# Performance work log

Measured on AMD Instinct MI355X. Metric: run time of the kernel, lower is better.

## Reference

```python
import jax, jax.numpy as jnp
import numpy as np

N, K, D, CP, H, S, P = 8192, 32, 768, 128, 8, 64, 8
NPTS = 3 * P  # 2*query_points + value_points = 24 points per head
FEAT = H * CP + H * S + H * P * 3 + H * P  # 1792


def layer_norm(x, scale, offset, eps=1e-5):
    m = x.mean(-1, keepdims=True)
    v = ((x - m) ** 2).mean(-1, keepdims=True)
    return (x - m) * jax.lax.rsqrt(v + eps) * scale + offset


def frames_from_pos(pos):
    # Gram-Schmidt rigid frame from backbone N(0), CA(1), C(2) atoms (extract_aa_frames).
    n, ca, c = pos[:, 0], pos[:, 1], pos[:, 2]
    eps = 1e-8
    v1 = c - ca
    v2 = n - ca
    e1 = v1 * jax.lax.rsqrt((v1 ** 2).sum(-1, keepdims=True) + eps)
    u2 = v2 - (v2 * e1).sum(-1, keepdims=True) * e1
    e2 = u2 * jax.lax.rsqrt((u2 ** 2).sum(-1, keepdims=True) + eps)
    e3 = jnp.cross(e1, e2)
    R = jnp.stack([e1, e2, e3], axis=-1)  # [N,3,3], columns = frame axes
    return R, ca


def setup_inputs() -> dict:
    key = jax.random.key(0)
    ks = jax.random.split(key, 10)
    inp = {
        "local": jax.random.normal(ks[0], (N, D), jnp.float32),
        "pos": jax.random.normal(ks[1], (N, 14, 3), jnp.float32) * 3.0,
        "pair": jax.random.normal(ks[2], (N, K, CP), jnp.float32),
        "pair_mask": jnp.ones((N, K), bool),
        "neighbours": jax.random.randint(ks[3], (N, K), 0, N, dtype=jnp.int32),
        "resi": jnp.arange(N, dtype=jnp.int32),
        "chain": jnp.zeros((N,), jnp.int32),
        "batch": jnp.zeros((N,), jnp.int32),
        "mask": jnp.ones((N,), bool),
        # parameters
        "ln_local_s": jnp.ones((D,), jnp.float32),
        "ln_local_b": jnp.zeros((D,), jnp.float32),
        "W_qkv": jax.random.normal(ks[4], (D, H * 3 * S), jnp.float32) / np.sqrt(D),
        "ln_q_s": jnp.ones((S,), jnp.float32),
        "ln_q_b": jnp.zeros((S,), jnp.float32),
        "ln_k_s": jnp.ones((S,), jnp.float32),
        "ln_k_b": jnp.zeros((S,), jnp.float32),
        "W_pts": jax.random.normal(ks[5], (D, H * NPTS * 3), jnp.float32) / np.sqrt(D),
        "W_bias": jax.random.normal(ks[6], (CP, H), jnp.float32) / np.sqrt(CP),
        "gamma": jnp.full((H,), np.log(np.e - 1.0), jnp.float32),
        "W_out": jax.random.normal(ks[7], (FEAT, D), jnp.float32) / np.sqrt(FEAT),
        "b_out": jnp.zeros((D,), jnp.float32),
    }
    return inp


def reference(local, pos, pair, pair_mask, neighbours, resi, chain, batch, mask,
              ln_local_s, ln_local_b, W_qkv, ln_q_s, ln_q_b, ln_k_s, ln_k_b,
              W_pts, W_bias, gamma, W_out, b_out):
    R, t = frames_from_pos(pos)                       # [N,3,3], [N,3]
    x = layer_norm(local, ln_local_s, ln_local_b)     # normalize=True
    qkv = (x @ W_qkv).reshape(-1, H, 3 * S)
    q, k, v = jnp.split(qkv, 3, axis=-1)              # each [N,H,S]
    q = layer_norm(q, ln_q_s, ln_q_b)
    k = layer_norm(k, ln_k_s, ln_k_b)
    # points in global frame: p = R @ raw + t
    raw = (x @ W_pts).reshape(-1, H, NPTS, 3)
    pts = jnp.einsum('nij,nhpj->nhpi', R, raw) + t[:, None, None]
    q_g, k_g, v_g = jnp.split(pts, [P, 2 * P], axis=-2)  # [N,H,P,3] each
    bias = jnp.einsum('nkc,ch->nkh', pair, W_bias)
    w_C = jnp.sqrt(2.0 / (9.0 * P))
    w_L = jnp.sqrt(1.0 / 3.0)
    dfactor = jax.nn.softplus(gamma)[None, None] * w_C / 2.0  # [1,1,H]
    diff = q_g[:, None] - k_g[neighbours]              # [N,K,H,P,3]
    dist = dfactor * (diff ** 2).sum((-1, -2))         # [N,K,H]
    dot = jnp.sqrt(1.0 / S) * jnp.einsum('nhc,nkhc->nkh', q, k[neighbours])
    logits = w_L * (dot + bias - dist)
    pm = pair_mask & (neighbours != -1)
    logits = jnp.where(pm[..., None], logits, -1e9)
    attn = jax.nn.softmax(logits, axis=1)              # softmax over neighbours (axis=-2)
    attn = jnp.where(pm[..., None], attn, 0.0)
    out_pair = jnp.einsum('nkh,nkc->nhc', attn, pair)
    out_scalar = jnp.einsum('nkh,nkhc->nhc', attn, v[neighbours])
    op = jnp.einsum('nkh,nkhpc->nhpc', attn, v_g[neighbours])
    # back to local frame: R^T (p - t)
    op = jnp.einsum('nji,nhpj->nhpi', R, op - t[:, None, None])
    out_norm = jnp.sqrt((op ** 2).sum(-1) + 1e-8)      # [N,H,P]
    Nn = local.shape[0]
    feats = jnp.concatenate([
        out_pair.reshape(Nn, -1), out_scalar.reshape(Nn, -1),
        op.reshape(Nn, -1), out_norm.reshape(Nn, -1)], axis=-1)
    return feats @ W_out + b_out
```

## Files before the change

### kernel.cpp

```cpp
#include <hip/hip_runtime.h>
#include <hip/hip_bf16.h>


#define NN 8192
#define KNBR 32
#define DD 768
#define CPC 128
#define HH 8
#define FEATD 1792
#define QKVD 1536
#define PTSD 576
#define PAIR_ROW 4096

typedef __hip_bfloat16 bf16;
typedef __attribute__((ext_vector_type(8))) short s8;
typedef __attribute__((ext_vector_type(4))) float f4;
typedef __attribute__((ext_vector_type(4))) float fv4;

__device__ __forceinline__ float b2f(bf16 v) { return __bfloat162float(v); }
__device__ __forceinline__ bf16 f2b(float v) { return __float2bfloat16(v); }
__device__ __forceinline__ unsigned short f2u(float v) {
    bf16 h = __float2bfloat16(v);
    return *(unsigned short*)&h;
}
__device__ __forceinline__ void gl_lds16(const void* g, void* l) {
    __builtin_amdgcn_global_load_lds(
        (const __attribute__((address_space(1))) void*)g,
        (__attribute__((address_space(3))) void*)l, 16, 0, 0);
}

__global__ __launch_bounds__(256) void frames_kernel(const float* __restrict__ pos,
                                                     float* __restrict__ Rm,
                                                     float* __restrict__ tv) {
    int n = blockIdx.x * blockDim.x + threadIdx.x;
    if (n >= NN) return;
    const float* p = pos + (size_t)n * 42;
    float nx[3], ca[3], cc[3];
#pragma unroll
    for (int j = 0; j < 3; ++j) { nx[j] = p[j]; ca[j] = p[3+j]; cc[j] = p[6+j]; }
    float v1[3], v2[3], e1[3], e2[3], e3[3];
#pragma unroll
    for (int j = 0; j < 3; ++j) { v1[j] = cc[j] - ca[j]; v2[j] = nx[j] - ca[j]; }
    float s1 = v1[0]*v1[0] + v1[1]*v1[1] + v1[2]*v1[2];
    float r1 = 1.0f / sqrtf(s1 + 1e-8f);
#pragma unroll
    for (int j = 0; j < 3; ++j) e1[j] = v1[j] * r1;
    float d = v2[0]*e1[0] + v2[1]*e1[1] + v2[2]*e1[2];
    float u2[3];
#pragma unroll
    for (int j = 0; j < 3; ++j) u2[j] = v2[j] - d * e1[j];
    float s2 = u2[0]*u2[0] + u2[1]*u2[1] + u2[2]*u2[2];
    float r2 = 1.0f / sqrtf(s2 + 1e-8f);
#pragma unroll
    for (int j = 0; j < 3; ++j) e2[j] = u2[j] * r2;
    e3[0] = e1[1]*e2[2] - e1[2]*e2[1];
    e3[1] = e1[2]*e2[0] - e1[0]*e2[2];
    e3[2] = e1[0]*e2[1] - e1[1]*e2[0];
#pragma unroll
    for (int i = 0; i < 3; ++i) {
        Rm[(size_t)n*9 + i*3 + 0] = e1[i];
        Rm[(size_t)n*9 + i*3 + 1] = e2[i];
        Rm[(size_t)n*9 + i*3 + 2] = e3[i];
        tv[(size_t)n*3 + i] = ca[i];
    }
}

__global__ __launch_bounds__(256) void ln_apply_kernel(const float* __restrict__ local,
                                                       const float* __restrict__ lns,
                                                       const float* __restrict__ lnb,
                                                       bf16* __restrict__ xln) {
    int n = blockIdx.x, tid = threadIdx.x;
    const float* row = local + (size_t)n * DD;
    float v[3];
#pragma unroll
    for (int e = 0; e < 3; ++e) v[e] = row[tid + 256*e];
    __shared__ float red[256];
    red[tid] = v[0] + v[1] + v[2];
    __syncthreads();
    for (int st = 128; st > 0; st >>= 1) {
        if (tid < st) red[tid] += red[tid + st];
        __syncthreads();
    }
    float mean = red[0] * (1.0f / DD);
    __syncthreads();
    float d0 = v[0]-mean, d1 = v[1]-mean, d2 = v[2]-mean;
    red[tid] = d0*d0 + d1*d1 + d2*d2;
    __syncthreads();
    for (int st = 128; st > 0; st >>= 1) {
        if (tid < st) red[tid] += red[tid + st];
        __syncthreads();
    }
    float rstd = rsqrtf(red[0] * (1.0f / DD) + 1e-5f);
    bf16* orow = xln + (size_t)n * DD;
#pragma unroll
    for (int e = 0; e < 3; ++e) {
        int c = tid + 256*e;
        orow[c] = f2b((v[e] - mean) * rstd * lns[c] + lnb[c]);
    }
}

__global__ __launch_bounds__(256) void transpose_kernel(const float* __restrict__ W,
                                                        bf16* __restrict__ Wt,
                                                        int K, int N,
                                                        int group, int cn, int segsz,
                                                        int rowoff) {
    __shared__ bf16 tile[32][33];
    int n0 = blockIdx.x * 32, k0 = blockIdx.y * 32;
    int tid = threadIdx.x;
    int r = tid >> 5, c = tid & 31;
    for (int rr = r; rr < 32; rr += 8) {
        int n = n0 + c;
        tile[rr][c] = (n < N) ? f2b(W[(size_t)(k0 + rr) * N + n]) : f2b(0.0f);
    }
    __syncthreads();
    for (int rr = r; rr < 32; rr += 8) {
        int n = n0 + rr;
        int pn = n;
        if (cn != 0 && n < N) {
            int hh = n / group, rm = n % group;
            pn = (rm / cn) * segsz + hh * cn + (rm % cn);
        }
        Wt[(size_t)(rowoff + pn) * K + k0 + c] = tile[c][rr];
    }
}

template<int SPLIT, int BIAS>
__global__ __launch_bounds__(256) void mfma_gemm(const bf16* __restrict__ A, int lda,
                                                 const bf16* __restrict__ Bt, int K,
                                                 void* __restrict__ C,
                                                 void* __restrict__ C2,
                                                 int ldc, int ncols,
                                                 const float* __restrict__ bias) {
    __shared__ short As[128 * 32];
    __shared__ short Bs[128 * 32];
    int tid = threadIdx.x;
    int w = tid >> 6, lane = tid & 63;
    int q = lane >> 4, lr = lane & 15;
    int m0 = blockIdx.y * 128, n0 = blockIdx.x * 128;
    int lrow = lane >> 2, lcol = (lane & 3) * 8;

    f4 acc[4][4] = {};

    for (int k0 = 0; k0 < K; k0 += 32) {
#pragma unroll
        for (int i = 0; i < 2; ++i) {
            int c = w * 2 + i;
            int r = c * 16 + lrow;
            gl_lds16(A  + (size_t)(m0 + r) * lda + k0 + lcol, As + c * 512);
            gl_lds16(Bt + (size_t)(n0 + r) * K   + k0 + lcol, Bs + c * 512);
        }
        __syncthreads();

        const short* Ab = As + ((w & 1) * 64 + lr) * 32 + q * 8;
        const short* Bb = Bs + ((w >> 1) * 64 + lr) * 32 + q * 8;
        s8 af[4], bfr[4];
#pragma unroll
        for (int i = 0; i < 4; ++i) af[i] = *(const s8*)(Ab + i * 16 * 32);
#pragma unroll
        for (int j = 0; j < 4; ++j) bfr[j] = *(const s8*)(Bb + j * 16 * 32);
#pragma unroll
        for (int i = 0; i < 4; ++i)
#pragma unroll
            for (int j = 0; j < 4; ++j)
                acc[i][j] = __builtin_amdgcn_mfma_f32_16x16x32_bf16(
                    af[i], bfr[j], acc[i][j], 0, 0, 0);
        __syncthreads();
    }

    int mb = m0 + (w & 1) * 64, nb = n0 + (w >> 1) * 64;
#pragma unroll
    for (int i = 0; i < 4; ++i) {
#pragma unroll
        for (int j = 0; j < 4; ++j) {
            int col = nb + j * 16 + lr;
            int row0 = mb + i * 16 + q * 4;
            if (!SPLIT) {
                if (col < ncols) {
#pragma unroll
                    for (int r = 0; r < 4; ++r) {
                        float v = acc[i][j][r];
                        if (BIAS) v += bias[col];
                        ((float*)C)[(size_t)(row0 + r) * ldc + col] = v;
                    }
                }
            } else {
                if (col < QKVD) {
#pragma unroll
                    for (int r = 0; r < 4; ++r)
                        ((unsigned short*)C)[(size_t)(row0 + r) * QKVD + col] =
                            f2u(acc[i][j][r]);
                } else if (col - QKVD < PTSD) {
                    int pc = col - QKVD;
#pragma unroll
                    for (int r = 0; r < 4; ++r)
                        ((float*)C2)[(size_t)(row0 + r) * PTSD + pc] = acc[i][j][r];
                }
            }
        }
    }
}

__global__ __launch_bounds__(256) void ln_qk_kernel(bf16* __restrict__ qkv,
                                                    const float* __restrict__ qs,
                                                    const float* __restrict__ qb,
                                                    const float* __restrict__ ks,
                                                    const float* __restrict__ kb) {
    int tid = threadIdx.x;
    int pi = blockIdx.x * 4 + (tid >> 6);
    int lane = tid & 63;
    bf16* base = qkv + (size_t)(pi >> 3) * QKVD + (pi & 7) * 64;
#pragma unroll
    for (int part = 0; part < 2; ++part) {
        int off = part * 512;
        const float* sc = part ? ks : qs;
        const float* of = part ? kb : qb;
        float v = b2f(base[off + lane]);
        float s = v;
#pragma unroll
        for (int m = 32; m > 0; m >>= 1) s += __shfl_xor(s, m, 64);
        float mean = s * (1.0f / 64.0f);
        float d = v - mean;
        float sq = d * d;
#pragma unroll
        for (int m = 32; m > 0; m >>= 1) sq += __shfl_xor(sq, m, 64);
        float inv = rsqrtf(sq * (1.0f / 64.0f) + 1e-5f);
        base[off + lane] = f2b(d * inv * sc[lane] + of[lane]);
    }
}

__global__ __launch_bounds__(256) void rotate_pts_kernel(float* __restrict__ pts,
                                                         const float* __restrict__ Rm,
                                                         const float* __restrict__ tv) {
    int idx = blockIdx.x * blockDim.x + threadIdx.x;
    if (idx >= NN * 192) return;
    int n = idx / 192;
    int rem = idx % 192;
    float* base = pts + (size_t)n * PTSD + rem * 3;
    float r0 = base[0], r1 = base[1], r2 = base[2];
    const float* R = Rm + (size_t)n * 9;
    const float* t = tv + (size_t)n * 3;
    base[0] = R[0]*r0 + R[1]*r1 + R[2]*r2 + t[0];
    base[1] = R[3]*r0 + R[4]*r1 + R[5]*r2 + t[1];
    base[2] = R[6]*r0 + R[7]*r1 + R[8]*r2 + t[2];
}

__global__ __launch_bounds__(256) void attn_kernel(const bf16* __restrict__ qkv,
                                                   const float* __restrict__ pts,
                                                   const float* __restrict__ Rm,
                                                   const float* __restrict__ tv,
                                                   float* __restrict__ pair,
                                                   const int* __restrict__ nbr,
                                                   const float* __restrict__ Wb,
                                                   const float* __restrict__ gamma) {
    int n = blockIdx.x;
    int tid = threadIdx.x;
    int w = tid >> 6, lane = tid & 63;
    int h = lane >> 3, cg = lane & 7;

    __shared__ float pairS[32][132];
    __shared__ float logitS[32][8];
    __shared__ float attnS[32][8];
    __shared__ float gS[192];
    __shared__ int nbS[32];
    __shared__ float dfS[8];

    const fv4* pr4 = (const fv4*)(pair + (size_t)n * PAIR_ROW);
    for (int e = tid; e < 1024; e += 256) {
        fv4 u = __builtin_nontemporal_load(pr4 + e);
        int k = e >> 5, c0 = (e & 31) * 4;
        *(fv4*)&pairS[k][c0] = u;
    }
    if (tid < 32) nbS[tid] = nbr[(size_t)n * KNBR + tid];
    if (tid < 8) dfS[tid] = log1pf(expf(gamma[tid])) * (1.0f / 12.0f);

    float qreg[8];
    {
        uint4 qv = *(const uint4*)(qkv + (size_t)n * QKVD + h * 64 + cg * 8);
        const unsigned short* qs = (const unsigned short*)&qv;
#pragma unroll
        for (int j = 0; j < 8; ++j) qreg[j] = b2f(*(const bf16*)&qs[j]);
    }
    fv4 qg = (fv4)(0.0f);
    if (cg < 6) qg = *(const fv4*)(pts + (size_t)n * PTSD + h * 24 + cg * 4);
    float wb[16];
#pragma unroll
    for (int j = 0; j < 16; ++j) wb[j] = Wb[(cg + 8 * j) * 8 + h];

    __syncthreads();

#pragma unroll
    for (int kk = 0; kk < 8; ++kk) {
        int k = w * 8 + kk;
        int nb = nbS[k];
        uint4 kv = *(const uint4*)(qkv + (size_t)nb * QKVD + 512 + h * 64 + cg * 8);
        const unsigned short* ks = (const unsigned short*)&kv;
        float dot = 0.0f;
#pragma unroll
        for (int j = 0; j < 8; ++j) dot += qreg[j] * b2f(*(const bf16*)&ks[j]);
        float d2 = 0.0f;
        if (cg < 6) {
            fv4 kg = *(const fv4*)(pts + (size_t)nb * PTSD + 192 + h * 24 + cg * 4);
            float dx = qg.x - kg.x, dy = qg.y - kg.y, dz = qg.z - kg.z, dw = qg.w - kg.w;
            d2 = dx*dx + dy*dy + dz*dz + dw*dw;
        }
        float bias = 0.0f;
#pragma unroll
        for (int j = 0; j < 16; ++j) bias += pairS[k][cg + 8 * j] * wb[j];

        float val = 0.125f * dot + bias - dfS[h] * d2;
        val += __shfl_xor(val, 1, 64);
        val += __shfl_xor(val, 2, 64);
        val += __shfl_xor(val, 4, 64);
        if (cg == 0) logitS[k][h] = 0.5773502691896258f * val;
    }
    __syncthreads();

    if (tid < 64) {
        int hh = tid >> 3, j = tid & 7;
        float l[4];
        float m = -1e30f;
#pragma unroll
        for (int i = 0; i < 4; ++i) { l[i] = logitS[j + 8 * i][hh]; m = fmaxf(m, l[i]); }
        m = fmaxf(m, __shfl_xor(m, 1, 64));
        m = fmaxf(m, __shfl_xor(m, 2, 64));
        m = fmaxf(m, __shfl_xor(m, 4, 64));
        float s = 0.0f;
#pragma unroll
        for (int i = 0; i < 4; ++i) { l[i] = expf(l[i] - m); s += l[i]; }
        s += __shfl_xor(s, 1, 64);
        s += __shfl_xor(s, 2, 64);
        s += __shfl_xor(s, 4, 64);
        float inv = 1.0f / s;
#pragma unroll
        for (int i = 0; i < 4; ++i) attnS[j + 8 * i][hh] = l[i] * inv;
    }
    __syncthreads();

    bf16* fr = (bf16*)(pair + (size_t)n * PAIR_ROW);
    for (int e = tid; e < 1024; e += 256) {
        int hh = e >> 7, c = e & 127;
        float acc = 0.0f;
#pragma unroll
        for (int k = 0; k < KNBR; ++k) acc += attnS[k][hh] * pairS[k][c];
        fr[e] = f2b(acc);
    }
    for (int e = tid; e < 512; e += 256) {
        int hh = e >> 6, c = e & 63;
        float acc = 0.0f;
#pragma unroll
        for (int k = 0; k < KNBR; ++k)
            acc += attnS[k][hh] * b2f(qkv[(size_t)nbS[k] * QKVD + 1024 + hh * 64 + c]);
        fr[1024 + e] = f2b(acc);
    }
    if (tid < 192) {
        int hh = tid / 24;
        float acc = 0.0f;
#pragma unroll
        for (int k = 0; k < KNBR; ++k)
            acc += attnS[k][hh] * pts[(size_t)nbS[k] * PTSD + 384 + tid];
        gS[tid] = acc;
    }
    __syncthreads();
    if (tid < 64) {
        int hh = tid >> 3, p = tid & 7;
        const float* t = tv + (size_t)n * 3;
        const float* R = Rm + (size_t)n * 9;
        float gx = gS[hh * 24 + p * 3 + 0] - t[0];
        float gy = gS[hh * 24 + p * 3 + 1] - t[1];
        float gz = gS[hh * 24 + p * 3 + 2] - t[2];
        float o0 = R[0]*gx + R[3]*gy + R[6]*gz;
        float o1 = R[1]*gx + R[4]*gy + R[7]*gz;
        float o2 = R[2]*gx + R[5]*gy + R[8]*gz;
        fr[1536 + hh*24 + p*3 + 0] = f2b(o0);
        fr[1536 + hh*24 + p*3 + 1] = f2b(o1);
        fr[1536 + hh*24 + p*3 + 2] = f2b(o2);
        fr[1728 + hh*8 + p] = f2b(sqrtf(o0*o0 + o1*o1 + o2*o2 + 1e-8f));
    }
}

extern "C" void kernel_launch(void* const* d_in, const int* in_sizes, int n_in,
                              void* d_out, int out_size, void* d_ws, size_t ws_size,
                              hipStream_t stream) {
    const float* local      = (const float*)d_in[0];
    const float* pos        = (const float*)d_in[1];
    float*       pair       = (float*)d_in[2];
    const int*   neighbours = (const int*)d_in[4];
    const float* ln_s   = (const float*)d_in[9];
    const float* ln_b   = (const float*)d_in[10];
    const float* W_qkv  = (const float*)d_in[11];
    const float* ln_q_s = (const float*)d_in[12];
    const float* ln_q_b = (const float*)d_in[13];
    const float* ln_k_s = (const float*)d_in[14];
    const float* ln_k_b = (const float*)d_in[15];
    const float* W_pts  = (const float*)d_in[16];
    const float* W_bias = (const float*)d_in[17];
    const float* gamma  = (const float*)d_in[18];
    const float* W_out  = (const float*)d_in[19];
    const float* b_out  = (const float*)d_in[20];
    float* out = (float*)d_out;

    float* Rm   = (float*)d_ws;
    float* tv   = Rm   + (size_t)NN * 9;
    float* pts  = tv   + (size_t)NN * 3;
    bf16*  qkv  = (bf16*)(pts + (size_t)NN * PTSD);
    bf16*  xln  = (bf16*)d_out;
    bf16*  wtm  = xln + (size_t)NN * DD;
    bf16*  wt3  = (bf16*)pts;

    frames_kernel<<<NN / 256, 256, 0, stream>>>(pos, Rm, tv);
    ln_apply_kernel<<<NN, 256, 0, stream>>>(local, ln_s, ln_b, xln);

    transpose_kernel<<<dim3(1536 / 32, 768 / 32), 256, 0, stream>>>(
        W_qkv, wtm, 768, 1536, 192, 64, 512, 0);
    transpose_kernel<<<dim3(640 / 32, 768 / 32), 256, 0, stream>>>(
        W_pts, wtm, 768, PTSD, 72, 24, 192, 1536);

    mfma_gemm<1, 0><<<dim3(2176 / 128, NN / 128), 256, 0, stream>>>(
        xln, DD, wtm, DD, qkv, pts, 0, 2176, nullptr);

    ln_qk_kernel<<<(NN * HH) / 4, 256, 0, stream>>>(qkv, ln_q_s, ln_q_b, ln_k_s, ln_k_b);
    rotate_pts_kernel<<<(NN * 192) / 256, 256, 0, stream>>>(pts, Rm, tv);

    attn_kernel<<<NN, 256, 0, stream>>>(qkv, pts, Rm, tv, pair, neighbours,
                                        W_bias, gamma);

    transpose_kernel<<<dim3(768 / 32, 1792 / 32), 256, 0, stream>>>(
        W_out, wt3, FEATD, DD, 0, 0, 0, 0);
    mfma_gemm<0, 1><<<dim3(768 / 128, NN / 128), 256, 0, stream>>>(
        (const bf16*)pair, PAIR_ROW * 2, wt3, FEATD, out, nullptr, DD, DD, b_out);
}
```

Before: 526.6 us.

## Fuse prep kernels, fold q/k layernorm into GEMM epilogue, vectorize pair aggregation

Frames, input layernorm and both weight transposes are merged into one prep launch, so four kernel launches become one. The separate q/k layernorm pass is removed: it now runs in the QKV GEMM epilogue using cross-lane shuffles over each 64-wide head tile, which saves a read-modify-write of the qkv buffer. The pair-feature aggregation in attention now computes four channels per thread with packed bf16 stores. The trade-offs are more divergent epilogue code and layernorm statistics taken from fp32 accumulators rather than from bf16-rounded values.

```diff
diff --git a/kernel.cpp b/kernel.cpp
--- a/kernel.cpp
+++ b/kernel.cpp
@@ -29,11 +29,9 @@
         (__attribute__((address_space(3))) void*)l, 16, 0, 0);
 }
 
-__global__ __launch_bounds__(256) void frames_kernel(const float* __restrict__ pos,
-                                                     float* __restrict__ Rm,
-                                                     float* __restrict__ tv) {
-    int n = blockIdx.x * blockDim.x + threadIdx.x;
-    if (n >= NN) return;
+__device__ __forceinline__ void do_frames(int n, const float* __restrict__ pos,
+                                          float* __restrict__ Rm,
+                                          float* __restrict__ tv) {
     const float* p = pos + (size_t)n * 42;
     float nx[3], ca[3], cc[3];
 #pragma unroll
@@ -65,48 +63,14 @@
     }
 }
 
-__global__ __launch_bounds__(256) void ln_apply_kernel(const float* __restrict__ local,
-                                                       const float* __restrict__ lns,
-                                                       const float* __restrict__ lnb,
-                                                       bf16* __restrict__ xln) {
-    int n = blockIdx.x, tid = threadIdx.x;
-    const float* row = local + (size_t)n * DD;
-    float v[3];
-#pragma unroll
-    for (int e = 0; e < 3; ++e) v[e] = row[tid + 256*e];
-    __shared__ float red[256];
-    red[tid] = v[0] + v[1] + v[2];
-    __syncthreads();
-    for (int st = 128; st > 0; st >>= 1) {
-        if (tid < st) red[tid] += red[tid + st];
-        __syncthreads();
-    }
-    float mean = red[0] * (1.0f / DD);
-    __syncthreads();
-    float d0 = v[0]-mean, d1 = v[1]-mean, d2 = v[2]-mean;
-    red[tid] = d0*d0 + d1*d1 + d2*d2;
-    __syncthreads();
-    for (int st = 128; st > 0; st >>= 1) {
-        if (tid < st) red[tid] += red[tid + st];
-        __syncthreads();
-    }
-    float rstd = rsqrtf(red[0] * (1.0f / DD) + 1e-5f);
-    bf16* orow = xln + (size_t)n * DD;
-#pragma unroll
-    for (int e = 0; e < 3; ++e) {
-        int c = tid + 256*e;
-        orow[c] = f2b((v[e] - mean) * rstd * lns[c] + lnb[c]);
-    }
-}
-
-__global__ __launch_bounds__(256) void transpose_kernel(const float* __restrict__ W,
-                                                        bf16* __restrict__ Wt,
-                                                        int K, int N,
-                                                        int group, int cn, int segsz,
-                                                        int rowoff) {
-    __shared__ bf16 tile[32][33];
-    int n0 = blockIdx.x * 32, k0 = blockIdx.y * 32;
-    int tid = threadIdx.x;
+__device__ __forceinline__ void do_transpose(const float* __restrict__ W,
+                                             bf16* __restrict__ Wt,
+                                             int K, int N, int group, int cn,
+                                             int segsz, int rowoff,
+                                             int bx, int by, int tid,
+                                             char* shbuf) {
+    bf16 (*tile)[33] = (bf16(*)[33])shbuf;
+    int n0 = bx * 32, k0 = by * 32;
     int r = tid >> 5, c = tid & 31;
     for (int rr = r; rr < 32; rr += 8) {
         int n = n0 + c;
@@ -124,13 +88,76 @@
     }
 }
 
+__global__ __launch_bounds__(256) void prep_kernel(
+        const float* __restrict__ local, const float* __restrict__ lns,
+        const float* __restrict__ lnb, bf16* __restrict__ xln,
+        const float* __restrict__ pos, float* __restrict__ Rm,
+        float* __restrict__ tv,
+        const float* __restrict__ W_qkv, const float* __restrict__ W_pts,
+        bf16* __restrict__ wtm) {
+    __shared__ __align__(16) char shbuf[2560];
+    int b = blockIdx.x, tid = threadIdx.x;
+    if (b < NN) {
+        if (b < 32) do_frames(b * 256 + tid, pos, Rm, tv);
+        float* red = (float*)shbuf;
+        const float* row = local + (size_t)b * DD;
+        float v[3];
+#pragma unroll
+        for (int e = 0; e < 3; ++e) v[e] = row[tid + 256*e];
+        red[tid] = v[0] + v[1] + v[2];
+        __syncthreads();
+        for (int st = 128; st > 0; st >>= 1) {
+            if (tid < st) red[tid] += red[tid + st];
+            __syncthreads();
+        }
+        float mean = red[0] * (1.0f / DD);
+        __syncthreads();
+        float d0 = v[0]-mean, d1 = v[1]-mean, d2 = v[2]-mean;
+        red[tid] = d0*d0 + d1*d1 + d2*d2;
+        __syncthreads();
+        for (int st = 128; st > 0; st >>= 1) {
+            if (tid < st) red[tid] += red[tid + st];
+            __syncthreads();
+        }
+        float rstd = rsqrtf(red[0] * (1.0f / DD) + 1e-5f);
+        bf16* orow = xln + (size_t)b * DD;
+#pragma unroll
+        for (int e = 0; e < 3; ++e) {
+            int c = tid + 256*e;
+            orow[c] = f2b((v[e] - mean) * rstd * lns[c] + lnb[c]);
+        }
+    } else if (b < NN + 1152) {
+        int t = b - NN;
+        do_transpose(W_qkv, wtm, 768, 1536, 192, 64, 512, 0, t % 48, t / 48,
+                     tid, shbuf);
+    } else {
+        int t = b - NN - 1152;
+        do_transpose(W_pts, wtm, 768, PTSD, 72, 24, 192, 1536, t % 20, t / 20,
+                     tid, shbuf);
+    }
+}
+
+__global__ __launch_bounds__(256) void transpose_kernel(const float* __restrict__ W,
+                                                        bf16* __restrict__ Wt,
+                                                        int K, int N,
+                                                        int group, int cn, int segsz,
+                                                        int rowoff) {
+    __shared__ __align__(16) char shbuf[2560];
+    do_transpose(W, Wt, K, N, group, cn, segsz, rowoff,
+                 blockIdx.x, blockIdx.y, threadIdx.x, shbuf);
+}
+
 template<int SPLIT, int BIAS>
 __global__ __launch_bounds__(256) void mfma_gemm(const bf16* __restrict__ A, int lda,
                                                  const bf16* __restrict__ Bt, int K,
                                                  void* __restrict__ C,
                                                  void* __restrict__ C2,
                                                  int ldc, int ncols,
-                                                 const float* __restrict__ bias) {
+                                                 const float* __restrict__ bias,
+                                                 const float* __restrict__ lnqs,
+                                                 const float* __restrict__ lnqb,
+                                                 const float* __restrict__ lnks,
+                                                 const float* __restrict__ lnkb) {
     __shared__ short As[128 * 32];
     __shared__ short Bs[128 * 32];
     int tid = threadIdx.x;
@@ -168,13 +195,13 @@
     }
 
     int mb = m0 + (w & 1) * 64, nb = n0 + (w >> 1) * 64;
-#pragma unroll
-    for (int i = 0; i < 4; ++i) {
-#pragma unroll
-        for (int j = 0; j < 4; ++j) {
-            int col = nb + j * 16 + lr;
-            int row0 = mb + i * 16 + q * 4;
-            if (!SPLIT) {
+    if (!SPLIT) {
+#pragma unroll
+        for (int i = 0; i < 4; ++i)
+#pragma unroll
+            for (int j = 0; j < 4; ++j) {
+                int col = nb + j * 16 + lr;
+                int row0 = mb + i * 16 + q * 4;
                 if (col < ncols) {
 #pragma unroll
                     for (int r = 0; r < 4; ++r) {
@@ -183,48 +210,61 @@
                         ((float*)C)[(size_t)(row0 + r) * ldc + col] = v;
                     }
                 }
-            } else {
-                if (col < QKVD) {
-#pragma unroll
-                    for (int r = 0; r < 4; ++r)
-                        ((unsigned short*)C)[(size_t)(row0 + r) * QKVD + col] =
-                            f2u(acc[i][j][r]);
-                } else if (col - QKVD < PTSD) {
+            }
+    } else if (nb < 1024) {
+        const float* sc = (nb < 512) ? lnqs : lnks;
+        const float* of = (nb < 512) ? lnqb : lnkb;
+        float scv[4], ofv[4];
+#pragma unroll
+        for (int j = 0; j < 4; ++j) { scv[j] = sc[j*16 + lr]; ofv[j] = of[j*16 + lr]; }
+#pragma unroll
+        for (int i = 0; i < 4; ++i) {
+#pragma unroll
+            for (int r = 0; r < 4; ++r) {
+                float s = acc[i][0][r] + acc[i][1][r] + acc[i][2][r] + acc[i][3][r];
+                s += __shfl_xor(s, 1, 64); s += __shfl_xor(s, 2, 64);
+                s += __shfl_xor(s, 4, 64); s += __shfl_xor(s, 8, 64);
+                float mean = s * (1.0f / 64.0f);
+                float d0 = acc[i][0][r] - mean, d1 = acc[i][1][r] - mean;
+                float d2 = acc[i][2][r] - mean, d3 = acc[i][3][r] - mean;
+                float vs = d0*d0 + d1*d1 + d2*d2 + d3*d3;
+                vs += __shfl_xor(vs, 1, 64); vs += __shfl_xor(vs, 2, 64);
+                vs += __shfl_xor(vs, 4, 64); vs += __shfl_xor(vs, 8, 64);
+                float rstd = rsqrtf(vs * (1.0f / 64.0f) + 1e-5f);
+                unsigned short* Crow =
+                    (unsigned short*)C + (size_t)(mb + i*16 + q*4 + r) * QKVD + nb;
+                Crow[0*16 + lr] = f2u(d0 * rstd * scv[0] + ofv[0]);
+                Crow[1*16 + lr] = f2u(d1 * rstd * scv[1] + ofv[1]);
+                Crow[2*16 + lr] = f2u(d2 * rstd * scv[2] + ofv[2]);
+                Crow[3*16 + lr] = f2u(d3 * rstd * scv[3] + ofv[3]);
+            }
+        }
+    } else if (nb < QKVD) {
+#pragma unroll
+        for (int i = 0; i < 4; ++i)
+#pragma unroll
+            for (int j = 0; j < 4; ++j) {
+                int col = nb + j * 16 + lr;
+                int row0 = mb + i * 16 + q * 4;
+#pragma unroll
+                for (int r = 0; r < 4; ++r)
+                    ((unsigned short*)C)[(size_t)(row0 + r) * QKVD + col] =
+                        f2u(acc[i][j][r]);
+            }
+    } else {
+#pragma unroll
+        for (int i = 0; i < 4; ++i)
+#pragma unroll
+            for (int j = 0; j < 4; ++j) {
+                int col = nb + j * 16 + lr;
+                int row0 = mb + i * 16 + q * 4;
+                if (col - QKVD < PTSD) {
                     int pc = col - QKVD;
 #pragma unroll
                     for (int r = 0; r < 4; ++r)
                         ((float*)C2)[(size_t)(row0 + r) * PTSD + pc] = acc[i][j][r];
                 }
             }
-        }
-    }
-}
-
-__global__ __launch_bounds__(256) void ln_qk_kernel(bf16* __restrict__ qkv,
-                                                    const float* __restrict__ qs,
-                                                    const float* __restrict__ qb,
-                                                    const float* __restrict__ ks,
-                                                    const float* __restrict__ kb) {
-    int tid = threadIdx.x;
-    int pi = blockIdx.x * 4 + (tid >> 6);
-    int lane = tid & 63;
-    bf16* base = qkv + (size_t)(pi >> 3) * QKVD + (pi & 7) * 64;
-#pragma unroll
-    for (int part = 0; part < 2; ++part) {
-        int off = part * 512;
-        const float* sc = part ? ks : qs;
-        const float* of = part ? kb : qb;
-        float v = b2f(base[off + lane]);
-        float s = v;
-#pragma unroll
-        for (int m = 32; m > 0; m >>= 1) s += __shfl_xor(s, m, 64);
-        float mean = s * (1.0f / 64.0f);
-        float d = v - mean;
-        float sq = d * d;
-#pragma unroll
-        for (int m = 32; m > 0; m >>= 1) sq += __shfl_xor(sq, m, 64);
-        float inv = rsqrtf(sq * (1.0f / 64.0f) + 1e-5f);
-        base[off + lane] = f2b(d * inv * sc[lane] + of[lane]);
     }
 }
 
@@ -337,12 +377,20 @@
     __syncthreads();
 
     bf16* fr = (bf16*)(pair + (size_t)n * PAIR_ROW);
-    for (int e = tid; e < 1024; e += 256) {
-        int hh = e >> 7, c = e & 127;
-        float acc = 0.0f;
-#pragma unroll
-        for (int k = 0; k < KNBR; ++k) acc += attnS[k][hh] * pairS[k][c];
-        fr[e] = f2b(acc);
+    {
+        int hh = tid >> 5;
+        int c4 = (tid & 31) * 4;
+        float a0 = 0.0f, a1 = 0.0f, a2 = 0.0f, a3 = 0.0f;
+#pragma unroll
+        for (int k = 0; k < KNBR; ++k) {
+            fv4 p = *(const fv4*)&pairS[k][c4];
+            float a = attnS[k][hh];
+            a0 += a * p.x; a1 += a * p.y; a2 += a * p.z; a3 += a * p.w;
+        }
+        unsigned int lo = (unsigned int)f2u(a0) | ((unsigned int)f2u(a1) << 16);
+        unsigned int hi = (unsigned int)f2u(a2) | ((unsigned int)f2u(a3) << 16);
+        uint2 pk; pk.x = lo; pk.y = hi;
+        *(uint2*)(fr + hh * 128 + c4) = pk;
     }
     for (int e = tid; e < 512; e += 256) {
         int hh = e >> 6, c = e & 63;
@@ -407,18 +455,13 @@
     bf16*  wtm  = xln + (size_t)NN * DD;
     bf16*  wt3  = (bf16*)pts;
 
-    frames_kernel<<<NN / 256, 256, 0, stream>>>(pos, Rm, tv);
-    ln_apply_kernel<<<NN, 256, 0, stream>>>(local, ln_s, ln_b, xln);
-
-    transpose_kernel<<<dim3(1536 / 32, 768 / 32), 256, 0, stream>>>(
-        W_qkv, wtm, 768, 1536, 192, 64, 512, 0);
-    transpose_kernel<<<dim3(640 / 32, 768 / 32), 256, 0, stream>>>(
-        W_pts, wtm, 768, PTSD, 72, 24, 192, 1536);
+    prep_kernel<<<NN + 1152 + 480, 256, 0, stream>>>(
+        local, ln_s, ln_b, xln, pos, Rm, tv, W_qkv, W_pts, wtm);
 
     mfma_gemm<1, 0><<<dim3(2176 / 128, NN / 128), 256, 0, stream>>>(
-        xln, DD, wtm, DD, qkv, pts, 0, 2176, nullptr);
-
-    ln_qk_kernel<<<(NN * HH) / 4, 256, 0, stream>>>(qkv, ln_q_s, ln_q_b, ln_k_s, ln_k_b);
+        xln, DD, wtm, DD, qkv, pts, 0, 2176, nullptr,
+        ln_q_s, ln_q_b, ln_k_s, ln_k_b);
+
     rotate_pts_kernel<<<(NN * 192) / 256, 256, 0, stream>>>(pts, Rm, tv);
 
     attn_kernel<<<NN, 256, 0, stream>>>(qkv, pts, Rm, tv, pair, neighbours,
@@ -427,5 +470,6 @@
     transpose_kernel<<<dim3(768 / 32, 1792 / 32), 256, 0, stream>>>(
         W_out, wt3, FEATD, DD, 0, 0, 0, 0);
     mfma_gemm<0, 1><<<dim3(768 / 128, NN / 128), 256, 0, stream>>>(
-        (const bf16*)pair, PAIR_ROW * 2, wt3, FEATD, out, nullptr, DD, DD, b_out);
-}
+        (const bf16*)pair, PAIR_ROW * 2, wt3, FEATD, out, nullptr, DD, DD, b_out,
+        nullptr, nullptr, nullptr, nullptr);
+}
```

After: 500.3 us. -5.0%, faster.
